# Kernel tuning notes

Hardware: AMD Instinct MI355X
Metric: run time of the kernel (lower is better)

Reference implementation:

```python
import jax, jax.numpy as jnp
import numpy as np


def setup_inputs() -> dict:
    key = jax.random.key(0)
    x = jax.random.normal(key, (8, 4096, 1024), dtype=jnp.float32)
    return {"x": x}


def reference(x) -> jnp.ndarray:
    # Faithful to the flax module: causal mask of zeros/-inf -> softmax ->
    # row i has uniform weights 1/(i+1) over positions 0..i, then attn @ x.
    B, T, C = x.shape
    tril = jnp.tril(jnp.ones((T, T), dtype=jnp.float32))
    attn = jnp.where(tril == 0, -jnp.inf, jnp.zeros((T, T), dtype=jnp.float32))
    attn = jax.nn.softmax(attn, axis=-1)  # [T, T], row i = 1/(i+1) on [0..i]
    # broadcast matmul over batch: [T,T] x [B,T,C] -> [B,T,C]
    return jnp.einsum('ts,bsc->btc', attn, x)
```

## Files before the change

### kernel.cpp

```cpp
#include <hip/hip_runtime.h>
#include <stdint.h>

namespace {

constexpr int kB      = 8;
constexpr int kT      = 4096;
constexpr int kC4     = 256;
constexpr int kNSeg   = 64;
constexpr int kSegLen = 64;
constexpr int kCols   = kB * kC4;
constexpr size_t kPartF4 = (size_t)kB * kNSeg * kC4;

__global__ __launch_bounds__(256) void seg_sum_kernel(const float4* __restrict__ x,
                                                      float4* __restrict__ part) {
    const int tid = blockIdx.x * 256 + threadIdx.x;
    const int c4  = tid & (kC4 - 1);
    const int seg = (tid >> 8) & (kNSeg - 1);
    const int b   = tid >> 14;

    const float4* p = x + ((size_t)(b * kT + seg * kSegLen)) * kC4 + c4;
    float sx = 0.f, sy = 0.f, sz = 0.f, sw = 0.f;
#pragma unroll 8
    for (int i = 0; i < kSegLen; ++i) {
        const float4 v = p[(size_t)i * kC4];
        sx += v.x; sy += v.y; sz += v.z; sw += v.w;
    }
    part[tid] = make_float4(sx, sy, sz, sw);
}

__global__ __launch_bounds__(64) void seg_prefix_kernel(const float4* __restrict__ part,
                                                        float4* __restrict__ excl) {
    const int col = blockIdx.x * 64 + threadIdx.x;
    const int c4  = col & (kC4 - 1);
    const int b   = col >> 8;
    const float4* p = part + (size_t)b * kNSeg * kC4 + c4;
    float4*       e = excl + (size_t)b * kNSeg * kC4 + c4;
    float rx = 0.f, ry = 0.f, rz = 0.f, rw = 0.f;
#pragma unroll 8
    for (int s = 0; s < kNSeg; ++s) {
        const float4 v = p[(size_t)s * kC4];
        e[(size_t)s * kC4] = make_float4(rx, ry, rz, rw);
        rx += v.x; ry += v.y; rz += v.z; rw += v.w;
    }
}

__global__ __launch_bounds__(256) void scan_write_kernel(const float4* __restrict__ x,
                                                         const float4* __restrict__ excl,
                                                         float4* __restrict__ out) {
    const int tid = blockIdx.x * 256 + threadIdx.x;
    const int c4  = tid & (kC4 - 1);
    const int seg = (tid >> 8) & (kNSeg - 1);
    const int b   = tid >> 14;

    const float4 o4 = excl[tid];
    float ox = o4.x, oy = o4.y, oz = o4.z, ow = o4.w;

    const size_t base = ((size_t)(b * kT + seg * kSegLen)) * kC4 + c4;
    const float4* p = x + base;
    float4* o       = out + base;
    const int t0    = seg * kSegLen;
#pragma unroll 4
    for (int i = 0; i < kSegLen; ++i) {
        const float4 v = p[(size_t)i * kC4];
        ox += v.x; oy += v.y; oz += v.z; ow += v.w;
        const float inv = __builtin_amdgcn_rcpf((float)(t0 + i + 1));
        o[(size_t)i * kC4] = make_float4(ox * inv, oy * inv, oz * inv, ow * inv);
    }
}

}

extern "C" void kernel_launch(void* const* d_in, const int* in_sizes, int n_in,
                              void* d_out, int out_size, void* d_ws, size_t ws_size,
                              hipStream_t stream) {
    const float4* x = (const float4*)d_in[0];
    float4* out     = (float4*)d_out;
    float4* part    = (float4*)d_ws;
    float4* excl    = part + kPartF4;
    constexpr int total = kB * kNSeg * kC4;
    seg_sum_kernel<<<total / 256, 256, 0, stream>>>(x, part);
    seg_prefix_kernel<<<kCols / 64, 64, 0, stream>>>(part, excl);
    scan_write_kernel<<<total / 256, 256, 0, stream>>>(x, excl, out);
}
```

Before: 70.01 us.

## Fuse three-pass segmented scan into one cooperative kernel with grid sync

Replaces the three-kernel scan (segment sums, prefix over segments, rescan and write) with a single cooperative kernel. Each block computes its segment sum, the blocks meet at a grid-wide barrier, then each block adds up all preceding segment sums itself before rescanning and writing. Output stores become nontemporal. This removes two launches and the separate prefix pass, at the cost of a grid barrier, a quadratic per-segment read of partial sums, and a fallback path if the cooperative launch fails.

```diff
diff --git a/kernel.cpp b/kernel.cpp
--- a/kernel.cpp
+++ b/kernel.cpp
@@ -1,15 +1,60 @@
 #include <hip/hip_runtime.h>
+#include <hip/hip_cooperative_groups.h>
 #include <stdint.h>
 
+namespace cg = cooperative_groups;
+
 namespace {
-
 constexpr int kB      = 8;
 constexpr int kT      = 4096;
 constexpr int kC4     = 256;
-constexpr int kNSeg   = 64;
 constexpr int kSegLen = 64;
-constexpr int kCols   = kB * kC4;
-constexpr size_t kPartF4 = (size_t)kB * kNSeg * kC4;
+constexpr int kNSeg   = kT / kSegLen;
+constexpr int kTiles  = kB * kNSeg;
+constexpr size_t kPartF4 = (size_t)kTiles * kC4;
+
+typedef float f4 __attribute__((ext_vector_type(4)));
+}
+
+__global__ __launch_bounds__(256) void coop_scan(const float4* __restrict__ x,
+                                                 float4* __restrict__ out,
+                                                 float4* __restrict__ vals) {
+    const int tile = (int)blockIdx.x;
+    const int b    = tile >> 6;
+    const int seg  = tile & (kNSeg - 1);
+    const int c4   = (int)threadIdx.x;
+
+    const size_t base = ((size_t)(b * kT + seg * kSegLen)) * kC4 + c4;
+    const float4* p = x + base;
+    float sx = 0.f, sy = 0.f, sz = 0.f, sw = 0.f;
+#pragma unroll 8
+    for (int i = 0; i < kSegLen; ++i) {
+        const float4 v = p[(size_t)i * kC4];
+        sx += v.x; sy += v.y; sz += v.z; sw += v.w;
+    }
+    vals[((size_t)tile << 8) + c4] = make_float4(sx, sy, sz, sw);
+
+    cg::this_grid().sync();
+
+    float ox = 0.f, oy = 0.f, oz = 0.f, ow = 0.f;
+#pragma unroll 4
+    for (int s = 0; s < seg; ++s) {
+        const float4 v = vals[((size_t)((b << 6) | s) << 8) + c4];
+        ox += v.x; oy += v.y; oz += v.z; ow += v.w;
+    }
+
+    f4* o = (f4*)(out + base);
+    const int t0 = seg * kSegLen;
+#pragma unroll 4
+    for (int i = 0; i < kSegLen; ++i) {
+        const float4 v = p[(size_t)i * kC4];
+        ox += v.x; oy += v.y; oz += v.z; ow += v.w;
+        const float inv = __builtin_amdgcn_rcpf((float)(t0 + i + 1));
+        f4 r;
+        r.x = ox * inv; r.y = oy * inv; r.z = oz * inv; r.w = ow * inv;
+        __builtin_nontemporal_store(r, o + (size_t)i * kC4);
+    }
+}
 
 __global__ __launch_bounds__(256) void seg_sum_kernel(const float4* __restrict__ x,
                                                       float4* __restrict__ part) {
@@ -17,7 +62,6 @@
     const int c4  = tid & (kC4 - 1);
     const int seg = (tid >> 8) & (kNSeg - 1);
     const int b   = tid >> 14;
-
     const float4* p = x + ((size_t)(b * kT + seg * kSegLen)) * kC4 + c4;
     float sx = 0.f, sy = 0.f, sz = 0.f, sw = 0.f;
 #pragma unroll 8
@@ -51,23 +95,21 @@
     const int c4  = tid & (kC4 - 1);
     const int seg = (tid >> 8) & (kNSeg - 1);
     const int b   = tid >> 14;
-
     const float4 o4 = excl[tid];
     float ox = o4.x, oy = o4.y, oz = o4.z, ow = o4.w;
-
     const size_t base = ((size_t)(b * kT + seg * kSegLen)) * kC4 + c4;
     const float4* p = x + base;
-    float4* o       = out + base;
-    const int t0    = seg * kSegLen;
+    f4* o = (f4*)(out + base);
+    const int t0 = seg * kSegLen;
 #pragma unroll 4
     for (int i = 0; i < kSegLen; ++i) {
         const float4 v = p[(size_t)i * kC4];
         ox += v.x; oy += v.y; oz += v.z; ow += v.w;
         const float inv = __builtin_amdgcn_rcpf((float)(t0 + i + 1));
-        o[(size_t)i * kC4] = make_float4(ox * inv, oy * inv, oz * inv, ow * inv);
+        f4 r;
+        r.x = ox * inv; r.y = oy * inv; r.z = oz * inv; r.w = ow * inv;
+        __builtin_nontemporal_store(r, o + (size_t)i * kC4);
     }
-}
-
 }
 
 extern "C" void kernel_launch(void* const* d_in, const int* in_sizes, int n_in,
@@ -75,10 +117,16 @@
                               hipStream_t stream) {
     const float4* x = (const float4*)d_in[0];
     float4* out     = (float4*)d_out;
-    float4* part    = (float4*)d_ws;
-    float4* excl    = part + kPartF4;
-    constexpr int total = kB * kNSeg * kC4;
-    seg_sum_kernel<<<total / 256, 256, 0, stream>>>(x, part);
-    seg_prefix_kernel<<<kCols / 64, 64, 0, stream>>>(part, excl);
-    scan_write_kernel<<<total / 256, 256, 0, stream>>>(x, excl, out);
+    float4* vals    = (float4*)d_ws;
+    void* args[] = { (void*)&x, (void*)&out, (void*)&vals };
+    hipError_t err = hipLaunchCooperativeKernel((const void*)coop_scan, dim3(kTiles),
+                                                dim3(256), args, 0, stream);
+    if (err != hipSuccess) {
+        float4* part = (float4*)d_ws;
+        float4* excl = part + kPartF4;
+        constexpr int total = kB * kNSeg * kC4;
+        seg_sum_kernel<<<total / 256, 256, 0, stream>>>(x, part);
+        seg_prefix_kernel<<<kB * kC4 / 64, 64, 0, stream>>>(part, excl);
+        scan_write_kernel<<<total / 256, 256, 0, stream>>>(x, excl, out);
+    }
 }
```

Measured after the change: 127.0 us. +81.4%, slower.
